# Optimization experiments

Hardware: AMD Instinct MI355X
Metric: run time of the kernel (lower is better)

## Reference

```python
import jax, jax.numpy as jnp
import numpy as np

SEQ = 4096
D = 1024


def setup_inputs() -> dict:
    key = jax.random.key(0)
    kx, kq, kk, kv = jax.random.split(key, 4)
    x = jax.random.normal(kx, (SEQ, D), dtype=jnp.float32)
    W_Q = jax.random.normal(kq, (D, D), dtype=jnp.float32)
    W_K = jax.random.normal(kk, (D, D), dtype=jnp.float32)
    W_V = jax.random.normal(kv, (D, D), dtype=jnp.float32)
    b_Q = jnp.zeros((D,), dtype=jnp.float32)
    b_K = jnp.zeros((D,), dtype=jnp.float32)
    b_V = jnp.zeros((D,), dtype=jnp.float32)
    return {"x": x, "W_Q": W_Q, "W_K": W_K, "W_V": W_V,
            "b_Q": b_Q, "b_K": b_K, "b_V": b_V}


def reference(x, W_Q, W_K, W_V, b_Q, b_K, b_V):
    d_head = W_Q.shape[0]
    q = x @ W_Q + b_Q                      # [S, D]
    k = x @ W_K + b_K                      # [S, D]
    v = x @ W_V + b_V                      # [S, D]
    scores = (q @ k.T) / jnp.sqrt(jnp.float32(d_head))  # [S, S]
    probs = jax.nn.softmax(scores, axis=-1)              # softmax over last axis
    return probs @ v                        # [S, D]
```

## Files before the change

### kernel.cpp

```cpp
#include <hip/hip_runtime.h>
#include <hip/hip_bf16.h>
#include <stdint.h>

#define SEQLEN 4096
#define DMODEL 1024

typedef uint16_t u16;
typedef uint32_t u32;

typedef __bf16 bf16x8 __attribute__((ext_vector_type(8)));
typedef float  f32x4  __attribute__((ext_vector_type(4)));
typedef u16    u16x8  __attribute__((ext_vector_type(8)));
typedef u16    u16x4  __attribute__((ext_vector_type(4)));

__device__ __forceinline__ u16 f2bf(float f) {
  union { float f; u32 u; } a; a.f = f;
  return (u16)((a.u + 0x7FFFu + ((a.u >> 16) & 1u)) >> 16);
}
__device__ __forceinline__ float bf2f(u16 h) {
  union { u32 u; float f; } a; a.u = ((u32)h) << 16;
  return a.f;
}

__device__ __forceinline__ void gl_lds16(const u16* g, u16* l) {
  __builtin_amdgcn_global_load_lds(
      (const __attribute__((address_space(1))) void*)g,
      (__attribute__((address_space(3))) void*)l,
      16, 0, 0);
}

__device__ __forceinline__ void stage64(const u16* __restrict__ g, int ld,
                                        int row0, int k0, u16* lds, int tid) {
#pragma unroll
  for (int it = 0; it < 4; ++it) {
    int u = tid + 256 * it;
    int row = u >> 3;
    int cg = (u & 7) ^ (row & 7);
    gl_lds16(g + (size_t)(row0 + row) * ld + (size_t)(k0 + cg * 8), lds + u * 8);
  }
}
__device__ __forceinline__ void stage32(const u16* __restrict__ g, int ld,
                                        int row0, int k0, u16* lds, int tid) {
#pragma unroll
  for (int it = 0; it < 2; ++it) {
    int u = tid + 256 * it;
    int row = u >> 2;
    int cg = (u & 3) ^ ((row >> 1) & 3);
    gl_lds16(g + (size_t)(row0 + row) * ld + (size_t)(k0 + cg * 8), lds + u * 8);
  }
}
__device__ __forceinline__ bf16x8 frag64(const u16* lds, int row, int chunk) {
  return *(const bf16x8*)(lds + row * 64 + ((chunk ^ (row & 7)) << 3));
}
__device__ __forceinline__ bf16x8 frag32(const u16* lds, int row, int chunk) {
  return *(const bf16x8*)(lds + row * 32 + ((chunk ^ ((row >> 1) & 3)) << 3));
}

#define MFMA16(c, a, b) c = __builtin_amdgcn_mfma_f32_16x16x32_bf16(a, b, c, 0, 0, 0)

__global__ void prep_kernel(const float* __restrict__ x,
                            const float* __restrict__ WQ,
                            const float* __restrict__ WK,
                            const float* __restrict__ WV,
                            u16* __restrict__ xh, u16* __restrict__ xl,
                            u16* __restrict__ wqh, u16* __restrict__ wql,
                            u16* __restrict__ wkh, u16* __restrict__ wkl,
                            u16* __restrict__ wvh, u16* __restrict__ wvl) {
  __shared__ float tile[64][65];
  int bx = blockIdx.x;
  if (bx < 768) {
    const float* W = (bx < 256) ? WQ : (bx < 512) ? WK : WV;
    u16* wth = (bx < 256) ? wqh : (bx < 512) ? wkh : wvh;
    u16* wtl = (bx < 256) ? wql : (bx < 512) ? wkl : wvl;
    int b = bx & 255;
    int n0 = (b & 15) * 64;
    int k0 = (b >> 4) * 64;
    int c = threadIdx.x & 63, r0 = threadIdx.x >> 6;
#pragma unroll
    for (int rr = 0; rr < 16; ++rr) {
      int r = r0 * 16 + rr;
      tile[r][c] = W[(size_t)(k0 + r) * DMODEL + n0 + c];
    }
    __syncthreads();
#pragma unroll
    for (int rr = 0; rr < 16; ++rr) {
      int n = r0 * 16 + rr;
      float f = tile[c][n];
      u16 hi = f2bf(f);
      wth[(size_t)(n0 + n) * DMODEL + k0 + c] = hi;
      wtl[(size_t)(n0 + n) * DMODEL + k0 + c] = f2bf(f - bf2f(hi));
    }
  } else {
    const int total = SEQLEN * DMODEL / 4;
    for (int idx = (bx - 768) * 256 + threadIdx.x; idx < total;
         idx += (gridDim.x - 768) * 256) {
      float4 f = ((const float4*)x)[idx];
      float ff[4] = {f.x, f.y, f.z, f.w};
      union { u16x4 v; u16 s[4]; } h, l;
#pragma unroll
      for (int uu = 0; uu < 4; ++uu) {
        u16 hi = f2bf(ff[uu]);
        h.s[uu] = hi;
        l.s[uu] = f2bf(ff[uu] - bf2f(hi));
      }
      ((u16x4*)xh)[idx] = h.v;
      ((u16x4*)xl)[idx] = l.v;
    }
  }
}

template <bool THREE, bool SPLITOUT>
__global__ __launch_bounds__(256, 4) void proj_kernel(
    const u16* __restrict__ Ah, const u16* __restrict__ Al,
    const u16* __restrict__ Bh, const u16* __restrict__ Bl,
    const float* __restrict__ bias, float scale,
    u16* __restrict__ outh, u16* __restrict__ outl, u16* __restrict__ outT) {
  __shared__ __align__(16) u16 st[16384];

  int tid = threadIdx.x;
  int lane = tid & 63, wid = tid >> 6;
  int wr = (wid >> 1) * 64, wc = (wid & 1) * 64;
  int r = lane & 15, g = lane >> 4;
  int m0 = blockIdx.x * 128, n0 = blockIdx.y * 128;

  f32x4 acc[4][4];
#pragma unroll
  for (int i = 0; i < 4; ++i)
#pragma unroll
    for (int j = 0; j < 4; ++j) acc[i][j] = (f32x4){0.f, 0.f, 0.f, 0.f};

  if (THREE) {
    for (int t = 0; t < DMODEL / 32; ++t) {
      int k0 = t * 32;
      __syncthreads();
      stage32(Ah, DMODEL, m0, k0, st + 0 * 4096, tid);
      stage32(Al, DMODEL, m0, k0, st + 1 * 4096, tid);
      stage32(Bh, DMODEL, n0, k0, st + 2 * 4096, tid);
      stage32(Bl, DMODEL, n0, k0, st + 3 * 4096, tid);
      __syncthreads();
      bf16x8 fa[4], fb[4], fal[4], fbl[4];
#pragma unroll
      for (int i = 0; i < 4; ++i) {
        fa[i]  = frag32(st + 0 * 4096, wr + i * 16 + r, g);
        fal[i] = frag32(st + 1 * 4096, wr + i * 16 + r, g);
        fb[i]  = frag32(st + 2 * 4096, wc + i * 16 + r, g);
        fbl[i] = frag32(st + 3 * 4096, wc + i * 16 + r, g);
      }
#pragma unroll
      for (int i = 0; i < 4; ++i)
#pragma unroll
        for (int j = 0; j < 4; ++j) {
          MFMA16(acc[i][j], fa[i], fb[j]);
          MFMA16(acc[i][j], fa[i], fbl[j]);
          MFMA16(acc[i][j], fal[i], fb[j]);
        }
    }
  } else {
    for (int t = 0; t < DMODEL / 64; ++t) {
      int k0 = t * 64;
      __syncthreads();
      stage64(Ah, DMODEL, m0, k0, st + 0 * 8192, tid);
      stage64(Bh, DMODEL, n0, k0, st + 1 * 8192, tid);
      __syncthreads();
#pragma unroll
      for (int ks = 0; ks < 2; ++ks) {
        bf16x8 fa[4], fb[4];
#pragma unroll
        for (int i = 0; i < 4; ++i) {
          fa[i] = frag64(st + 0 * 8192, wr + i * 16 + r, ks * 4 + g);
          fb[i] = frag64(st + 1 * 8192, wc + i * 16 + r, ks * 4 + g);
        }
#pragma unroll
        for (int i = 0; i < 4; ++i)
#pragma unroll
          for (int j = 0; j < 4; ++j) MFMA16(acc[i][j], fa[i], fb[j]);
      }
    }
  }

#pragma unroll
  for (int i = 0; i < 4; ++i)
#pragma unroll
    for (int j = 0; j < 4; ++j) {
      int col = n0 + wc + j * 16 + r;
      float bv = bias[col];
#pragma unroll
      for (int t = 0; t < 4; ++t) {
        int row = m0 + wr + i * 16 + g * 4 + t;
        float v = (acc[i][j][t] + bv) * scale;
        if (SPLITOUT) {
          u16 hi = f2bf(v);
          outh[(size_t)row * DMODEL + col] = hi;
          outl[(size_t)row * DMODEL + col] = f2bf(v - bf2f(hi));
        } else {
          outT[(size_t)col * SEQLEN + row] = f2bf(v);
        }
      }
    }
}

__global__ __launch_bounds__(256, 4) void scores_kernel(
    const u16* __restrict__ qh, const u16* __restrict__ ql,
    const u16* __restrict__ kh, const u16* __restrict__ kl,
    u16* __restrict__ P, float* __restrict__ mloc, float* __restrict__ tsum) {
  __shared__ __align__(16) u16 st[16384];
  __shared__ float sm_max[256];
  __shared__ float sm_sum[256];

  int tid = threadIdx.x;
  int lane = tid & 63, wid = tid >> 6;
  int wr = (wid >> 1) * 64, wc = (wid & 1) * 64;
  int r = lane & 15, g = lane >> 4;
  int halfid = wid & 1;
  int m0 = blockIdx.x * 128, n0 = blockIdx.y * 128;

  f32x4 acc[4][4];
#pragma unroll
  for (int i = 0; i < 4; ++i)
#pragma unroll
    for (int j = 0; j < 4; ++j) acc[i][j] = (f32x4){0.f, 0.f, 0.f, 0.f};

  for (int t = 0; t < DMODEL / 32; ++t) {
    int k0 = t * 32;
    __syncthreads();
    stage32(qh, DMODEL, m0, k0, st + 0 * 4096, tid);
    stage32(ql, DMODEL, m0, k0, st + 1 * 4096, tid);
    stage32(kh, DMODEL, n0, k0, st + 2 * 4096, tid);
    stage32(kl, DMODEL, n0, k0, st + 3 * 4096, tid);
    __syncthreads();
    bf16x8 fa[4], fb[4], fal[4], fbl[4];
#pragma unroll
    for (int i = 0; i < 4; ++i) {
      fa[i]  = frag32(st + 0 * 4096, wr + i * 16 + r, g);
      fal[i] = frag32(st + 1 * 4096, wr + i * 16 + r, g);
      fb[i]  = frag32(st + 2 * 4096, wc + i * 16 + r, g);
      fbl[i] = frag32(st + 3 * 4096, wc + i * 16 + r, g);
    }
#pragma unroll
    for (int i = 0; i < 4; ++i)
#pragma unroll
      for (int j = 0; j < 4; ++j) {
        MFMA16(acc[i][j], fa[i], fb[j]);
        MFMA16(acc[i][j], fa[i], fbl[j]);
        MFMA16(acc[i][j], fal[i], fb[j]);
      }
  }

  __syncthreads();

#pragma unroll
  for (int i = 0; i < 4; ++i)
#pragma unroll
    for (int t = 0; t < 4; ++t) {
      float m = fmaxf(fmaxf(acc[i][0][t], acc[i][1][t]),
                      fmaxf(acc[i][2][t], acc[i][3][t]));
      m = fmaxf(m, __shfl_xor(m, 1));
      m = fmaxf(m, __shfl_xor(m, 2));
      m = fmaxf(m, __shfl_xor(m, 4));
      m = fmaxf(m, __shfl_xor(m, 8));
      if (r == 0) sm_max[halfid * 128 + wr + i * 16 + g * 4 + t] = m;
    }
  __syncthreads();

#pragma unroll
  for (int i = 0; i < 4; ++i)
#pragma unroll
    for (int t = 0; t < 4; ++t) {
      int R = wr + i * 16 + g * 4 + t;
      float mx = fmaxf(sm_max[R], sm_max[128 + R]);
      int sw = ((R >> 2) & 3) << 5;
      float lsum = 0.f;
#pragma unroll
      for (int j = 0; j < 4; ++j) {
        float e = exp2f((acc[i][j][t] - mx) * 1.4426950408889634f);
        lsum += e;
        st[R * 128 + ((wc + j * 16 + r) ^ sw)] = f2bf(e);
      }
      lsum += __shfl_xor(lsum, 1);
      lsum += __shfl_xor(lsum, 2);
      lsum += __shfl_xor(lsum, 4);
      lsum += __shfl_xor(lsum, 8);
      if (r == 0) sm_sum[halfid * 128 + R] = lsum;
    }
  __syncthreads();

#pragma unroll
  for (int k = 0; k < 8; ++k) {
    int cidx = k * 256 + tid;
    int rrow = cidx >> 4;
    int col0 = (cidx & 15) * 8;
    int sw = ((rrow >> 2) & 3) << 5;
    u16x8 v = *(const u16x8*)(st + rrow * 128 + (col0 ^ sw));
    *(u16x8*)(P + (size_t)(m0 + rrow) * SEQLEN + n0 + col0) = v;
  }

  if (halfid == 0 && r == 0) {
#pragma unroll
    for (int i = 0; i < 4; ++i)
#pragma unroll
      for (int t = 0; t < 4; ++t) {
        int R = wr + i * 16 + g * 4 + t;
        int grow = m0 + R;
        mloc[(size_t)blockIdx.y * SEQLEN + grow] =
            fmaxf(sm_max[R], sm_max[128 + R]);
        tsum[(size_t)blockIdx.y * SEQLEN + grow] = sm_sum[R] + sm_sum[128 + R];
      }
  }
}

__global__ void finalize_kernel(const float* __restrict__ mloc,
                                const float* __restrict__ tsum,
                                float* __restrict__ rowscale) {
  int rr = blockIdx.x * 256 + threadIdx.x;
  if (rr >= SEQLEN) return;
  float M = -3.0e38f;
#pragma unroll
  for (int t = 0; t < 32; ++t) M = fmaxf(M, mloc[t * SEQLEN + rr]);
  float l = 0.f;
#pragma unroll
  for (int t = 0; t < 32; ++t)
    l += tsum[t * SEQLEN + rr] * exp2f((mloc[t * SEQLEN + rr] - M) * 1.4426950408889634f);
  float inv = 1.0f / l;
#pragma unroll
  for (int t = 0; t < 32; ++t)
    rowscale[t * SEQLEN + rr] = exp2f((mloc[t * SEQLEN + rr] - M) * 1.4426950408889634f) * inv;
}

__global__ void pnorm_kernel(u16* __restrict__ P, const float* __restrict__ rowscale) {
  const int total = SEQLEN * SEQLEN / 8;
  for (int idx = blockIdx.x * 256 + threadIdx.x; idx < total; idx += gridDim.x * 256) {
    int rrow = idx >> 9;
    int c8 = idx & 511;
    int t = c8 >> 4;
    float sc = rowscale[t * SEQLEN + rrow];
    union { u16x8 v; u16 s[8]; } d;
    d.v = ((u16x8*)P)[idx];
#pragma unroll
    for (int uu = 0; uu < 8; ++uu) d.s[uu] = f2bf(bf2f(d.s[uu]) * sc);
    ((u16x8*)P)[idx] = d.v;
  }
}

__global__ __launch_bounds__(256, 4) void pv_kernel(const u16* __restrict__ P,
                                                    const u16* __restrict__ vT,
                                                    float* __restrict__ out) {
  __shared__ __align__(16) u16 st[16384];
  int tid = threadIdx.x;
  int lane = tid & 63, wid = tid >> 6;
  int wr = (wid >> 1) * 64, wc = (wid & 1) * 64;
  int r = lane & 15, g = lane >> 4;
  int m0 = blockIdx.x * 128, n0 = blockIdx.y * 128;

  f32x4 acc[4][4];
#pragma unroll
  for (int i = 0; i < 4; ++i)
#pragma unroll
    for (int j = 0; j < 4; ++j) acc[i][j] = (f32x4){0.f, 0.f, 0.f, 0.f};

  for (int t = 0; t < SEQLEN / 64; ++t) {
    int k0 = t * 64;
    __syncthreads();
    stage64(P, SEQLEN, m0, k0, st + 0 * 8192, tid);
    stage64(vT, SEQLEN, n0, k0, st + 1 * 8192, tid);
    __syncthreads();
#pragma unroll
    for (int ks = 0; ks < 2; ++ks) {
      bf16x8 fa[4], fb[4];
#pragma unroll
      for (int i = 0; i < 4; ++i) {
        fa[i] = frag64(st + 0 * 8192, wr + i * 16 + r, ks * 4 + g);
        fb[i] = frag64(st + 1 * 8192, wc + i * 16 + r, ks * 4 + g);
      }
#pragma unroll
      for (int i = 0; i < 4; ++i)
#pragma unroll
        for (int j = 0; j < 4; ++j) MFMA16(acc[i][j], fa[i], fb[j]);
    }
  }
#pragma unroll
  for (int i = 0; i < 4; ++i)
#pragma unroll
    for (int j = 0; j < 4; ++j)
#pragma unroll
      for (int t = 0; t < 4; ++t)
        out[(size_t)(m0 + wr + i * 16 + g * 4 + t) * DMODEL + n0 + wc + j * 16 + r] =
            acc[i][j][t];
}

extern "C" void kernel_launch(void* const* d_in, const int* in_sizes, int n_in,
                              void* d_out, int out_size, void* d_ws, size_t ws_size,
                              hipStream_t stream) {
  (void)in_sizes; (void)n_in; (void)out_size; (void)ws_size;
  const float* x  = (const float*)d_in[0];
  const float* WQ = (const float*)d_in[1];
  const float* WK = (const float*)d_in[2];
  const float* WV = (const float*)d_in[3];
  const float* bQ = (const float*)d_in[4];
  const float* bK = (const float*)d_in[5];
  const float* bV = (const float*)d_in[6];
  float* out = (float*)d_out;
  char* ws = (char*)d_ws;
  const size_t MB = 1ull << 20;

  u16* xh   = (u16*)(ws + 0);
  u16* xl   = (u16*)(ws + 8 * MB);
  u16* wqh  = (u16*)(ws + 16 * MB);
  u16* wql  = (u16*)(ws + 18 * MB);
  u16* wkh  = (u16*)(ws + 20 * MB);
  u16* wkl  = (u16*)(ws + 22 * MB);
  u16* wvh  = (u16*)(ws + 24 * MB);
  u16* wvl  = (u16*)(ws + 26 * MB);
  u16* P    = (u16*)(ws + 0);
  u16* qh   = (u16*)(ws + 32 * MB);
  u16* ql   = (u16*)(ws + 40 * MB);
  u16* kh   = (u16*)(ws + 48 * MB);
  u16* kl   = (u16*)(ws + 56 * MB);
  u16* vT   = (u16*)(ws + 64 * MB);
  float* mloc     = (float*)(ws + 72 * MB);
  float* tsum     = (float*)(ws + 72 * MB + 512 * 1024);
  float* rowscale = (float*)(ws + 73 * MB);

  prep_kernel<<<2816, 256, 0, stream>>>(x, WQ, WK, WV, xh, xl, wqh, wql,
                                        wkh, wkl, wvh, wvl);

  dim3 gproj(32, 8);
  proj_kernel<true, true><<<gproj, 256, 0, stream>>>(xh, xl, wqh, wql, bQ,
                                                     1.0f / 32.0f, qh, ql, nullptr);
  proj_kernel<true, true><<<gproj, 256, 0, stream>>>(xh, xl, wkh, wkl, bK,
                                                     1.0f, kh, kl, nullptr);
  proj_kernel<false, false><<<gproj, 256, 0, stream>>>(xh, nullptr, wvh, nullptr, bV,
                                                       1.0f, nullptr, nullptr, vT);

  dim3 gsc(32, 32);
  scores_kernel<<<gsc, 256, 0, stream>>>(qh, ql, kh, kl, P, mloc, tsum);
  finalize_kernel<<<16, 256, 0, stream>>>(mloc, tsum, rowscale);
  pnorm_kernel<<<4096, 256, 0, stream>>>(P, rowscale);

  dim3 gpv(32, 8);
  pv_kernel<<<gpv, 256, 0, stream>>>(P, vT, out);
}
```

Baseline: 372.8 us.

## Double-buffer LDS staging in GEMM kernels and fuse P normalization into PV

Each GEMM-style kernel (projection, scores, PV) now uses two LDS buffers. The next k-tile's global-to-LDS loads are issued before the current tile's MFMAs, with a single vmcnt wait and barrier per iteration and raised wave priority around the MFMA block. The separate pnorm pass over the 4096x4096 P matrix is removed: PV loads per-row tile scales and applies them to the A fragments in registers. This doubles LDS use per block and lowers the launch-bounds occupancy hint from 4 to 2. It also adds per-element bf16 rescaling work inside the PV inner loop.

```diff
diff --git a/kernel.cpp b/kernel.cpp
--- a/kernel.cpp
+++ b/kernel.cpp
@@ -13,6 +13,9 @@
 typedef u16    u16x8  __attribute__((ext_vector_type(8)));
 typedef u16    u16x4  __attribute__((ext_vector_type(4)));
 
+#define VMCNT0() asm volatile("s_waitcnt vmcnt(0)" ::: "memory")
+#define BAR() __builtin_amdgcn_s_barrier()
+
 __device__ __forceinline__ u16 f2bf(float f) {
   union { float f; u32 u; } a; a.f = f;
   return (u16)((a.u + 0x7FFFu + ((a.u >> 16) & 1u)) >> 16);
@@ -20,6 +23,14 @@
 __device__ __forceinline__ float bf2f(u16 h) {
   union { u32 u; float f; } a; a.u = ((u32)h) << 16;
   return a.f;
+}
+
+union U8 { bf16x8 v; u16 s[8]; };
+__device__ __forceinline__ bf16x8 scale8(bf16x8 a, float s) {
+  U8 in, out; in.v = a;
+#pragma unroll
+  for (int e = 0; e < 8; ++e) out.s[e] = f2bf(bf2f(in.s[e]) * s);
+  return out.v;
 }
 
 __device__ __forceinline__ void gl_lds16(const u16* g, u16* l) {
@@ -110,12 +121,12 @@
 }
 
 template <bool THREE, bool SPLITOUT>
-__global__ __launch_bounds__(256, 4) void proj_kernel(
+__global__ __launch_bounds__(256, 2) void proj_kernel(
     const u16* __restrict__ Ah, const u16* __restrict__ Al,
     const u16* __restrict__ Bh, const u16* __restrict__ Bl,
     const float* __restrict__ bias, float scale,
     u16* __restrict__ outh, u16* __restrict__ outl, u16* __restrict__ outT) {
-  __shared__ __align__(16) u16 st[16384];
+  __shared__ __align__(16) u16 st[32768];
 
   int tid = threadIdx.x;
   int lane = tid & 63, wid = tid >> 6;
@@ -130,22 +141,32 @@
     for (int j = 0; j < 4; ++j) acc[i][j] = (f32x4){0.f, 0.f, 0.f, 0.f};
 
   if (THREE) {
-    for (int t = 0; t < DMODEL / 32; ++t) {
-      int k0 = t * 32;
-      __syncthreads();
-      stage32(Ah, DMODEL, m0, k0, st + 0 * 4096, tid);
-      stage32(Al, DMODEL, m0, k0, st + 1 * 4096, tid);
-      stage32(Bh, DMODEL, n0, k0, st + 2 * 4096, tid);
-      stage32(Bl, DMODEL, n0, k0, st + 3 * 4096, tid);
-      __syncthreads();
+    const int NT = DMODEL / 32;
+    stage32(Ah, DMODEL, m0, 0, st + 0 * 4096, tid);
+    stage32(Al, DMODEL, m0, 0, st + 1 * 4096, tid);
+    stage32(Bh, DMODEL, n0, 0, st + 2 * 4096, tid);
+    stage32(Bl, DMODEL, n0, 0, st + 3 * 4096, tid);
+    VMCNT0(); BAR();
+    int cur = 0;
+    for (int t = 0; t < NT; ++t) {
+      if (t + 1 < NT) {
+        int k0 = (t + 1) * 32;
+        u16* nb = st + (cur ^ 1) * 16384;
+        stage32(Ah, DMODEL, m0, k0, nb + 0 * 4096, tid);
+        stage32(Al, DMODEL, m0, k0, nb + 1 * 4096, tid);
+        stage32(Bh, DMODEL, n0, k0, nb + 2 * 4096, tid);
+        stage32(Bl, DMODEL, n0, k0, nb + 3 * 4096, tid);
+      }
+      const u16* cb = st + cur * 16384;
       bf16x8 fa[4], fb[4], fal[4], fbl[4];
 #pragma unroll
       for (int i = 0; i < 4; ++i) {
-        fa[i]  = frag32(st + 0 * 4096, wr + i * 16 + r, g);
-        fal[i] = frag32(st + 1 * 4096, wr + i * 16 + r, g);
-        fb[i]  = frag32(st + 2 * 4096, wc + i * 16 + r, g);
-        fbl[i] = frag32(st + 3 * 4096, wc + i * 16 + r, g);
-      }
+        fa[i]  = frag32(cb + 0 * 4096, wr + i * 16 + r, g);
+        fal[i] = frag32(cb + 1 * 4096, wr + i * 16 + r, g);
+        fb[i]  = frag32(cb + 2 * 4096, wc + i * 16 + r, g);
+        fbl[i] = frag32(cb + 3 * 4096, wc + i * 16 + r, g);
+      }
+      __builtin_amdgcn_s_setprio(1);
 #pragma unroll
       for (int i = 0; i < 4; ++i)
 #pragma unroll
@@ -154,27 +175,41 @@
           MFMA16(acc[i][j], fa[i], fbl[j]);
           MFMA16(acc[i][j], fal[i], fb[j]);
         }
+      __builtin_amdgcn_s_setprio(0);
+      VMCNT0(); BAR();
+      cur ^= 1;
     }
   } else {
-    for (int t = 0; t < DMODEL / 64; ++t) {
-      int k0 = t * 64;
-      __syncthreads();
-      stage64(Ah, DMODEL, m0, k0, st + 0 * 8192, tid);
-      stage64(Bh, DMODEL, n0, k0, st + 1 * 8192, tid);
-      __syncthreads();
+    const int NT = DMODEL / 64;
+    stage64(Ah, DMODEL, m0, 0, st + 0 * 8192, tid);
+    stage64(Bh, DMODEL, n0, 0, st + 1 * 8192, tid);
+    VMCNT0(); BAR();
+    int cur = 0;
+    for (int t = 0; t < NT; ++t) {
+      if (t + 1 < NT) {
+        int k0 = (t + 1) * 64;
+        u16* nb = st + (cur ^ 1) * 16384;
+        stage64(Ah, DMODEL, m0, k0, nb + 0 * 8192, tid);
+        stage64(Bh, DMODEL, n0, k0, nb + 1 * 8192, tid);
+      }
+      const u16* cb = st + cur * 16384;
+      __builtin_amdgcn_s_setprio(1);
 #pragma unroll
       for (int ks = 0; ks < 2; ++ks) {
         bf16x8 fa[4], fb[4];
 #pragma unroll
         for (int i = 0; i < 4; ++i) {
-          fa[i] = frag64(st + 0 * 8192, wr + i * 16 + r, ks * 4 + g);
-          fb[i] = frag64(st + 1 * 8192, wc + i * 16 + r, ks * 4 + g);
+          fa[i] = frag64(cb + 0 * 8192, wr + i * 16 + r, ks * 4 + g);
+          fb[i] = frag64(cb + 1 * 8192, wc + i * 16 + r, ks * 4 + g);
         }
 #pragma unroll
         for (int i = 0; i < 4; ++i)
 #pragma unroll
           for (int j = 0; j < 4; ++j) MFMA16(acc[i][j], fa[i], fb[j]);
       }
+      __builtin_amdgcn_s_setprio(0);
+      VMCNT0(); BAR();
+      cur ^= 1;
     }
   }
 
@@ -199,11 +234,11 @@
     }
 }
 
-__global__ __launch_bounds__(256, 4) void scores_kernel(
+__global__ __launch_bounds__(256, 2) void scores_kernel(
     const u16* __restrict__ qh, const u16* __restrict__ ql,
     const u16* __restrict__ kh, const u16* __restrict__ kl,
     u16* __restrict__ P, float* __restrict__ mloc, float* __restrict__ tsum) {
-  __shared__ __align__(16) u16 st[16384];
+  __shared__ __align__(16) u16 st[32768];
   __shared__ float sm_max[256];
   __shared__ float sm_sum[256];
 
@@ -220,22 +255,32 @@
 #pragma unroll
     for (int j = 0; j < 4; ++j) acc[i][j] = (f32x4){0.f, 0.f, 0.f, 0.f};
 
-  for (int t = 0; t < DMODEL / 32; ++t) {
-    int k0 = t * 32;
-    __syncthreads();
-    stage32(qh, DMODEL, m0, k0, st + 0 * 4096, tid);
-    stage32(ql, DMODEL, m0, k0, st + 1 * 4096, tid);
-    stage32(kh, DMODEL, n0, k0, st + 2 * 4096, tid);
-    stage32(kl, DMODEL, n0, k0, st + 3 * 4096, tid);
-    __syncthreads();
+  const int NT = DMODEL / 32;
+  stage32(qh, DMODEL, m0, 0, st + 0 * 4096, tid);
+  stage32(ql, DMODEL, m0, 0, st + 1 * 4096, tid);
+  stage32(kh, DMODEL, n0, 0, st + 2 * 4096, tid);
+  stage32(kl, DMODEL, n0, 0, st + 3 * 4096, tid);
+  VMCNT0(); BAR();
+  int cur = 0;
+  for (int t = 0; t < NT; ++t) {
+    if (t + 1 < NT) {
+      int k0 = (t + 1) * 32;
+      u16* nb = st + (cur ^ 1) * 16384;
+      stage32(qh, DMODEL, m0, k0, nb + 0 * 4096, tid);
+      stage32(ql, DMODEL, m0, k0, nb + 1 * 4096, tid);
+      stage32(kh, DMODEL, n0, k0, nb + 2 * 4096, tid);
+      stage32(kl, DMODEL, n0, k0, nb + 3 * 4096, tid);
+    }
+    const u16* cb = st + cur * 16384;
     bf16x8 fa[4], fb[4], fal[4], fbl[4];
 #pragma unroll
     for (int i = 0; i < 4; ++i) {
-      fa[i]  = frag32(st + 0 * 4096, wr + i * 16 + r, g);
-      fal[i] = frag32(st + 1 * 4096, wr + i * 16 + r, g);
-      fb[i]  = frag32(st + 2 * 4096, wc + i * 16 + r, g);
-      fbl[i] = frag32(st + 3 * 4096, wc + i * 16 + r, g);
-    }
+      fa[i]  = frag32(cb + 0 * 4096, wr + i * 16 + r, g);
+      fal[i] = frag32(cb + 1 * 4096, wr + i * 16 + r, g);
+      fb[i]  = frag32(cb + 2 * 4096, wc + i * 16 + r, g);
+      fbl[i] = frag32(cb + 3 * 4096, wc + i * 16 + r, g);
+    }
+    __builtin_amdgcn_s_setprio(1);
 #pragma unroll
     for (int i = 0; i < 4; ++i)
 #pragma unroll
@@ -244,6 +289,9 @@
         MFMA16(acc[i][j], fa[i], fbl[j]);
         MFMA16(acc[i][j], fal[i], fb[j]);
       }
+    __builtin_amdgcn_s_setprio(0);
+    VMCNT0(); BAR();
+    cur ^= 1;
   }
 
   __syncthreads();
@@ -326,25 +374,10 @@
     rowscale[t * SEQLEN + rr] = exp2f((mloc[t * SEQLEN + rr] - M) * 1.4426950408889634f) * inv;
 }
 
-__global__ void pnorm_kernel(u16* __restrict__ P, const float* __restrict__ rowscale) {
-  const int total = SEQLEN * SEQLEN / 8;
-  for (int idx = blockIdx.x * 256 + threadIdx.x; idx < total; idx += gridDim.x * 256) {
-    int rrow = idx >> 9;
-    int c8 = idx & 511;
-    int t = c8 >> 4;
-    float sc = rowscale[t * SEQLEN + rrow];
-    union { u16x8 v; u16 s[8]; } d;
-    d.v = ((u16x8*)P)[idx];
-#pragma unroll
-    for (int uu = 0; uu < 8; ++uu) d.s[uu] = f2bf(bf2f(d.s[uu]) * sc);
-    ((u16x8*)P)[idx] = d.v;
-  }
-}
-
-__global__ __launch_bounds__(256, 4) void pv_kernel(const u16* __restrict__ P,
-                                                    const u16* __restrict__ vT,
-                                                    float* __restrict__ out) {
-  __shared__ __align__(16) u16 st[16384];
+__global__ __launch_bounds__(256, 2) void pv_kernel(
+    const u16* __restrict__ P, const u16* __restrict__ vT,
+    const float* __restrict__ rowscale, float* __restrict__ out) {
+  __shared__ __align__(16) u16 st[32768];
   int tid = threadIdx.x;
   int lane = tid & 63, wid = tid >> 6;
   int wr = (wid >> 1) * 64, wc = (wid & 1) * 64;
@@ -357,25 +390,43 @@
 #pragma unroll
     for (int j = 0; j < 4; ++j) acc[i][j] = (f32x4){0.f, 0.f, 0.f, 0.f};
 
-  for (int t = 0; t < SEQLEN / 64; ++t) {
-    int k0 = t * 64;
-    __syncthreads();
-    stage64(P, SEQLEN, m0, k0, st + 0 * 8192, tid);
-    stage64(vT, SEQLEN, n0, k0, st + 1 * 8192, tid);
-    __syncthreads();
+  const int NT = SEQLEN / 64;
+  stage64(P, SEQLEN, m0, 0, st + 0 * 8192, tid);
+  stage64(vT, SEQLEN, n0, 0, st + 1 * 8192, tid);
+  VMCNT0(); BAR();
+  int cur = 0;
+  float rs[4];
+  for (int t = 0; t < NT; ++t) {
+    if ((t & 1) == 0) {
+      int c = t >> 1;
+#pragma unroll
+      for (int i = 0; i < 4; ++i)
+        rs[i] = rowscale[(size_t)c * SEQLEN + m0 + wr + i * 16 + r];
+    }
+    if (t + 1 < NT) {
+      int k0 = (t + 1) * 64;
+      u16* nb = st + (cur ^ 1) * 16384;
+      stage64(P, SEQLEN, m0, k0, nb + 0 * 8192, tid);
+      stage64(vT, SEQLEN, n0, k0, nb + 1 * 8192, tid);
+    }
+    const u16* cb = st + cur * 16384;
 #pragma unroll
     for (int ks = 0; ks < 2; ++ks) {
       bf16x8 fa[4], fb[4];
 #pragma unroll
       for (int i = 0; i < 4; ++i) {
-        fa[i] = frag64(st + 0 * 8192, wr + i * 16 + r, ks * 4 + g);
-        fb[i] = frag64(st + 1 * 8192, wc + i * 16 + r, ks * 4 + g);
-      }
+        fa[i] = scale8(frag64(cb + 0 * 8192, wr + i * 16 + r, ks * 4 + g), rs[i]);
+        fb[i] = frag64(cb + 1 * 8192, wc + i * 16 + r, ks * 4 + g);
+      }
+      __builtin_amdgcn_s_setprio(1);
 #pragma unroll
       for (int i = 0; i < 4; ++i)
 #pragma unroll
         for (int j = 0; j < 4; ++j) MFMA16(acc[i][j], fa[i], fb[j]);
-    }
+      __builtin_amdgcn_s_setprio(0);
+    }
+    VMCNT0(); BAR();
+    cur ^= 1;
   }
 #pragma unroll
   for (int i = 0; i < 4; ++i)
@@ -434,8 +485,7 @@
   dim3 gsc(32, 32);
   scores_kernel<<<gsc, 256, 0, stream>>>(qh, ql, kh, kl, P, mloc, tsum);
   finalize_kernel<<<16, 256, 0, stream>>>(mloc, tsum, rowscale);
-  pnorm_kernel<<<4096, 256, 0, stream>>>(P, rowscale);
 
   dim3 gpv(32, 8);
-  pv_kernel<<<gpv, 256, 0, stream>>>(P, vT, out);
-}
+  pv_kernel<<<gpv, 256, 0, stream>>>(P, vT, rowscale, out);
+}
```

After: 359.6 us. 3.5% less time.
